# Performance work log

Measured on AMD Instinct MI355X. Metric: run time of the kernel, lower is better.

Reference implementation:

```python
import jax, jax.numpy as jnp
import numpy as np

B, C_LEN, Q_LEN, H = 32, 1024, 128, 512
NEG = -1e30  # effectively -inf for fp32 softmax


def setup_inputs() -> dict:
    key = jax.random.key(0)
    k1, k2, k3, k4, k5, k6 = jax.random.split(key, 6)
    C = jax.random.normal(k1, (B, C_LEN, H), dtype=jnp.float32)
    Q = jax.random.normal(k2, (B, Q_LEN, H), dtype=jnp.float32)
    C_mask = jax.random.randint(k3, (B, C_LEN), 0, 2, dtype=jnp.int32)
    Q_mask = jax.random.randint(k4, (B, Q_LEN), 0, 2, dtype=jnp.int32)
    # nn.Linear(3H, 1): weight [1, 3H], bias [1]; store as flat vector + scalar
    w = jax.random.normal(k5, (3 * H,), dtype=jnp.float32) * (1.0 / np.sqrt(3 * H))
    b = jax.random.normal(k6, (1,), dtype=jnp.float32) * 0.01
    return {"C": C, "Q": Q, "C_mask": C_mask, "Q_mask": Q_mask, "w": w, "b": b}


def reference(C, Q, C_mask, Q_mask, w, b):
    h = C.shape[-1]
    w1, w2, w3 = w[:h], w[h:2 * h], w[2 * h:]
    # Trilinear score decomposition (same math as Linear on cat(C, Q, C*Q)):
    # S[b,i,j] = C_i.w1 + Q_j.w2 + (C_i*w3).Q_j + bias
    S = (C @ w1)[:, :, None] + (Q @ w2)[:, None, :] \
        + jnp.einsum('bih,bjh->bij', C * w3, Q) + b[0]
    S_row = jax.nn.softmax(jnp.where(Q_mask[:, None, :] == 0, NEG, S), axis=2)
    S_col = jax.nn.softmax(jnp.where(C_mask[:, :, None] == 0, NEG, S), axis=1)
    A = jnp.einsum('bij,bjh->bih', S_row, Q)                     # [B, c_len, H]
    Bm = jnp.einsum('bij,bkj,bkh->bih', S_row, S_col, C)         # S_row @ S_col^T @ C
    return jnp.concatenate((C, A, C * A, C * Bm), axis=-1)       # [B, c_len, 4H]
```

## Files before the change

### kernel.cpp

```cpp
#include <hip/hip_runtime.h>
#include <hip/hip_bf16.h>
#include <math.h>

#define Bn 32
#define CL 1024
#define QL 128
#define Hh 512
#define NEGV (-1e30f)

typedef short bf16x8 __attribute__((ext_vector_type(8)));
typedef float f32x4 __attribute__((ext_vector_type(4)));

__device__ inline unsigned short f2bf(float x) {
  union { float f; unsigned u; } v; v.f = x;
  unsigned r = v.u + 0x7fff + ((v.u >> 16) & 1);
  return (unsigned short)(r >> 16);
}
__device__ inline unsigned packbf(float x, float y) {
  return (unsigned)f2bf(x) | ((unsigned)f2bf(y) << 16);
}

__global__ __launch_bounds__(256) void rowdot_kernel(
    const float* __restrict__ X, const float* __restrict__ w,
    const float* __restrict__ bias, float* __restrict__ out, int nrows) {
  int row = blockIdx.x * 4 + (threadIdx.x >> 6);
  int lane = threadIdx.x & 63;
  if (row >= nrows) return;
  const float* x = X + (size_t)row * Hh;
  float s = 0.f;
  for (int h = lane; h < Hh; h += 64) s += x[h] * w[h];
  for (int off = 32; off > 0; off >>= 1) s += __shfl_down(s, off, 64);
  if (lane == 0) out[row] = s + (bias ? bias[0] : 0.f);
}

__global__ __launch_bounds__(256) void prep_q_kernel(
    const float* __restrict__ Q, const float* __restrict__ w3,
    unsigned short* __restrict__ Qs, unsigned short* __restrict__ QT) {
  __shared__ float tile[QL * 65];
  int b = blockIdx.y, h0 = blockIdx.x * 64, t = threadIdx.x;
  const float* Qb = Q + (size_t)b * QL * Hh;
  unsigned* Qsu = (unsigned*)Qs + (size_t)b * QL * (Hh / 2);
  unsigned* QTu = (unsigned*)QT + ((size_t)b * Hh + h0) * (QL / 2);
  for (int l = 0; l < 16; ++l) {
    int idx = t + l * 256; int c = idx & 31, j = idx >> 5;
    float2 v = *(const float2*)(Qb + (size_t)j * Hh + h0 + 2 * c);
    float wa = w3[h0 + 2 * c], wb = w3[h0 + 2 * c + 1];
    Qsu[(size_t)j * (Hh / 2) + h0 / 2 + c] = packbf(v.x * wa, v.y * wb);
    tile[j * 65 + 2 * c] = v.x;
    tile[j * 65 + 2 * c + 1] = v.y;
  }
  __syncthreads();
  for (int l = 0; l < 16; ++l) {
    int idx = t + l * 256; int jc = idx & 63, h = idx >> 6;
    QTu[(size_t)h * (QL / 2) + jc] =
        packbf(tile[(2 * jc) * 65 + h], tile[(2 * jc + 1) * 65 + h]);
  }
}

__global__ __launch_bounds__(256) void s_mfma_kernel(
    const float* __restrict__ C, const unsigned short* __restrict__ Qs,
    const float* __restrict__ w1, const int* __restrict__ Qmask,
    const int* __restrict__ Cmask, const float* __restrict__ cq,
    float* __restrict__ S, unsigned short* __restrict__ Prow,
    unsigned short* __restrict__ C16,
    float* __restrict__ partm, float* __restrict__ partl) {
  __shared__ unsigned sA[64 * 32];
  __shared__ unsigned sB[128 * 32];
  __shared__ float rcs[64];
  __shared__ int qm[QL];
  __shared__ int cmk[64];
  __shared__ float swm[4 * QL], swl[4 * QL];
  int b = blockIdx.y, i0 = blockIdx.x * 64, t = threadIdx.x;
  if (t < QL) qm[t] = Qmask[b * QL + t];
  if (t >= 128 && t < 192) cmk[t - 128] = Cmask[b * CL + i0 + (t - 128)];
  __syncthreads();
  int lane = t & 63, w = t >> 6;
  int lanen = lane & 15, quad = lane >> 4;
  int rbase = t >> 5, cc = t & 31;
  f32x4 acc[8];
  for (int nt = 0; nt < 8; ++nt) acc[nt] = (f32x4){0.f, 0.f, 0.f, 0.f};
  float racc[8];
  for (int l = 0; l < 8; ++l) racc[l] = 0.f;
  const float* Cb = C + ((size_t)b * CL + i0) * Hh;
  unsigned* C16u = (unsigned*)C16 + ((size_t)b * CL + i0) * (Hh / 2);
  const unsigned* Qsu = (const unsigned*)Qs + (size_t)b * QL * (Hh / 2);
  for (int k0 = 0; k0 < Hh; k0 += 64) {
    float2 wv = *(const float2*)(w1 + k0 + 2 * cc);
    for (int l = 0; l < 8; ++l) {
      int rr = rbase + l * 8;
      float2 v = *(const float2*)(Cb + (size_t)rr * Hh + k0 + 2 * cc);
      unsigned pk = packbf(v.x, v.y);
      sA[rr * 32 + (cc ^ ((rr & 7) << 2))] = pk;
      C16u[(size_t)rr * (Hh / 2) + k0 / 2 + cc] = pk;
      racc[l] += v.x * wv.x + v.y * wv.y;
    }
    for (int l = 0; l < 16; ++l) {
      int idx = t + l * 256; int c = idx & 31, j = idx >> 5;
      sB[j * 32 + (c ^ ((j & 7) << 2))] = Qsu[(size_t)j * (Hh / 2) + k0 / 2 + c];
    }
    __syncthreads();
    for (int kk = 0; kk < 2; ++kk) {
      int arow = w * 16 + lanen;
      bf16x8 a = *(const bf16x8*)(sA + arow * 32 + ((kk * 16 + quad * 4) ^ ((arow & 7) << 2)));
      for (int nt = 0; nt < 8; ++nt) {
        int brow = nt * 16 + lanen;
        bf16x8 bb = *(const bf16x8*)(sB + brow * 32 + ((kk * 16 + quad * 4) ^ ((brow & 7) << 2)));
        acc[nt] = __builtin_amdgcn_mfma_f32_16x16x32_bf16(a, bb, acc[nt], 0, 0, 0);
      }
    }
    __syncthreads();
  }
  for (int l = 0; l < 8; ++l) {
    float s = racc[l];
    for (int off = 1; off <= 16; off <<= 1) s += __shfl_xor(s, off, 64);
    if (cc == 0) rcs[rbase + l * 8] = s;
  }
  __syncthreads();
  float cqv[8]; int qmv[8];
  for (int nt = 0; nt < 8; ++nt) {
    int j = nt * 16 + lanen;
    cqv[nt] = cq[b * QL + j];
    qmv[nt] = qm[j];
  }
  float colM[8], colL[8];
  for (int nt = 0; nt < 8; ++nt) { colM[nt] = -INFINITY; colL[nt] = 0.f; }
  int rowbase = i0 + w * 16 + quad * 4;
  for (int r = 0; r < 4; ++r) {
    int row = rowbase + r;
    float rcv = rcs[w * 16 + quad * 4 + r];
    int cmr = cmk[w * 16 + quad * 4 + r];
    float vals[8], mv = -INFINITY;
    for (int nt = 0; nt < 8; ++nt) {
      float val = acc[nt][r] + rcv + cqv[nt];
      vals[nt] = val;
      mv = fmaxf(mv, qmv[nt] ? val : NEGV);
    }
    for (int off = 1; off < 16; off <<= 1) mv = fmaxf(mv, __shfl_xor(mv, off, 64));
    float ls = 0.f;
    for (int nt = 0; nt < 8; ++nt) ls += __expf((qmv[nt] ? vals[nt] : NEGV) - mv);
    for (int off = 1; off < 16; off <<= 1) ls += __shfl_xor(ls, off, 64);
    float linv = 1.f / ls;
    size_t base = ((size_t)b * CL + row) * QL;
    for (int nt = 0; nt < 8; ++nt) {
      int j = nt * 16 + lanen;
      S[base + j] = vals[nt];
      Prow[base + j] = f2bf(__expf((qmv[nt] ? vals[nt] : NEGV) - mv) * linv);
      float v = cmr ? vals[nt] : NEGV;
      float nm = fmaxf(colM[nt], v);
      colL[nt] = colL[nt] * __expf(colM[nt] - nm) + __expf(v - nm);
      colM[nt] = nm;
    }
  }
  for (int off = 16; off <= 32; off <<= 1) {
    for (int nt = 0; nt < 8; ++nt) {
      float m2 = __shfl_xor(colM[nt], off, 64);
      float l2 = __shfl_xor(colL[nt], off, 64);
      float nm = fmaxf(colM[nt], m2);
      colL[nt] = colL[nt] * __expf(colM[nt] - nm) + l2 * __expf(m2 - nm);
      colM[nt] = nm;
    }
  }
  if (quad == 0) {
    for (int nt = 0; nt < 8; ++nt) {
      swm[w * QL + nt * 16 + lanen] = colM[nt];
      swl[w * QL + nt * 16 + lanen] = colL[nt];
    }
  }
  __syncthreads();
  if (t < QL) {
    float m = -INFINITY, L = 0.f;
    for (int ww = 0; ww < 4; ++ww) {
      float m2 = swm[ww * QL + t], l2 = swl[ww * QL + t];
      float nm = fmaxf(m, m2);
      L = L * __expf(m - nm) + l2 * __expf(m2 - nm);
      m = nm;
    }
    partm[((size_t)b * 16 + blockIdx.x) * QL + t] = m;
    partl[((size_t)b * 16 + blockIdx.x) * QL + t] = L;
  }
}

__global__ __launch_bounds__(128) void colstat2_kernel(
    const float* __restrict__ partm, const float* __restrict__ partl,
    float* __restrict__ colm, float* __restrict__ colinv) {
  int b = blockIdx.x, j = threadIdx.x;
  float m = -INFINITY, L = 0.f;
  for (int c = 0; c < 16; ++c) {
    float m2 = partm[(b * 16 + c) * QL + j], l2 = partl[(b * 16 + c) * QL + j];
    float nm = fmaxf(m, m2);
    L = L * __expf(m - nm) + l2 * __expf(m2 - nm);
    m = nm;
  }
  colm[b * QL + j] = m;
  colinv[b * QL + j] = 1.f / L;
}

__global__ __launch_bounds__(256) void pcol_kernel(
    const float* __restrict__ S, const int* __restrict__ Cmask,
    const float* __restrict__ colm, const float* __restrict__ colinv,
    unsigned short* __restrict__ PT) {
  __shared__ float tile[64 * 129];
  __shared__ int cm[64];
  __shared__ float cmj[QL], civ[QL];
  int b = blockIdx.y, i0 = blockIdx.x * 64, t = threadIdx.x;
  if (t < 64) cm[t] = Cmask[b * CL + i0 + t];
  if (t >= 128) { int j = t - 128; cmj[j] = colm[b * QL + j]; civ[j] = colinv[b * QL + j]; }
  __syncthreads();
  const float* Sb = S + ((size_t)b * CL + i0) * QL;
  for (int l = 0; l < 32; ++l) {
    int idx = t + l * 256; int j = idx & 127, il = idx >> 7;
    float v = cm[il] ? Sb[(size_t)il * QL + j] : NEGV;
    tile[il * 129 + j] = __expf(v - cmj[j]) * civ[j];
  }
  __syncthreads();
  unsigned* PTu = (unsigned*)PT;
  for (int l = 0; l < 16; ++l) {
    int idx = t + l * 256; int c = idx & 31, j = idx >> 5;
    PTu[(((size_t)b * QL + j) * CL + i0) / 2 + c] =
        packbf(tile[(2 * c) * 129 + j], tile[(2 * c + 1) * 129 + j]);
  }
}

__global__ __launch_bounds__(256) void t_mfma_kernel(
    const unsigned short* __restrict__ C16, const unsigned short* __restrict__ PT,
    unsigned short* __restrict__ TT) {
  __shared__ unsigned ct[64 * 17];
  __shared__ unsigned sA[32 * 32];
  __shared__ unsigned sB[128 * 32];
  int b = blockIdx.y, h0 = blockIdx.x * 32, t = threadIdx.x;
  int lane = t & 63, w = t >> 6;
  int lanen = lane & 15, quad = lane >> 4;
  int mw = w >> 1, nw = w & 1;
  f32x4 acc[4];
  for (int nt = 0; nt < 4; ++nt) acc[nt] = (f32x4){0.f, 0.f, 0.f, 0.f};
  const unsigned* C16u = (const unsigned*)C16 + (size_t)b * CL * (Hh / 2) + h0 / 2;
  const unsigned* PTu = (const unsigned*)PT + (size_t)b * QL * (CL / 2);
  const unsigned short* ct16 = (const unsigned short*)ct;
  for (int i0 = 0; i0 < CL; i0 += 64) {
    for (int l = 0; l < 4; ++l) {
      int idx = t + l * 256; int hc = idx & 15, ii = idx >> 4;
      ct[ii * 17 + hc] = C16u[(size_t)(i0 + ii) * (Hh / 2) + hc];
    }
    for (int l = 0; l < 16; ++l) {
      int idx = t + l * 256; int c = idx & 31, j = idx >> 5;
      sB[j * 32 + (c ^ ((j & 7) << 2))] = PTu[(size_t)j * (CL / 2) + i0 / 2 + c];
    }
    __syncthreads();
    for (int l = 0; l < 4; ++l) {
      int idx = t + l * 256; int c = idx & 31, hh = idx >> 5;
      unsigned lo = ct16[(2 * c) * 34 + hh];
      unsigned hi = ct16[(2 * c + 1) * 34 + hh];
      sA[hh * 32 + (c ^ ((hh & 7) << 2))] = lo | (hi << 16);
    }
    __syncthreads();
    for (int kk = 0; kk < 2; ++kk) {
      int arow = mw * 16 + lanen;
      bf16x8 a = *(const bf16x8*)(sA + arow * 32 + ((kk * 16 + quad * 4) ^ ((arow & 7) << 2)));
      for (int nt = 0; nt < 4; ++nt) {
        int brow = nw * 64 + nt * 16 + lanen;
        bf16x8 bb = *(const bf16x8*)(sB + brow * 32 + ((kk * 16 + quad * 4) ^ ((brow & 7) << 2)));
        acc[nt] = __builtin_amdgcn_mfma_f32_16x16x32_bf16(a, bb, acc[nt], 0, 0, 0);
      }
    }
    __syncthreads();
  }
  for (int nt = 0; nt < 4; ++nt)
    for (int r = 0; r < 4; ++r) {
      int h = h0 + mw * 16 + quad * 4 + r;
      int j = nw * 64 + nt * 16 + lanen;
      TT[((size_t)b * Hh + h) * QL + j] = f2bf(acc[nt][r]);
    }
}

__global__ __launch_bounds__(256) void out_mfma_kernel(
    const unsigned short* __restrict__ Prow, const unsigned short* __restrict__ TT,
    const unsigned short* __restrict__ QT, const float* __restrict__ C,
    float* __restrict__ out) {
  __shared__ unsigned sP[64 * 64];
  __shared__ unsigned sQ[64 * 64];
  __shared__ unsigned sT[64 * 64];
  int b = blockIdx.z, i0 = blockIdx.y * 64, h0 = blockIdx.x * 64, t = threadIdx.x;
  int lane = t & 63, w = t >> 6;
  int lanen = lane & 15, quad = lane >> 4;
  const unsigned* Pu = (const unsigned*)Prow + ((size_t)b * CL + i0) * (QL / 2);
  const unsigned* Tu = (const unsigned*)TT + ((size_t)b * Hh + h0) * (QL / 2);
  const unsigned* Qu = (const unsigned*)QT + ((size_t)b * Hh + h0) * (QL / 2);
  for (int l = 0; l < 16; ++l) {
    int idx = t + l * 256; int c = idx & 63, rr = idx >> 6;
    int cs = c ^ ((rr & 7) << 2);
    sP[rr * 64 + cs] = Pu[(size_t)rr * 64 + c];
    sQ[rr * 64 + cs] = Qu[(size_t)rr * 64 + c];
    sT[rr * 64 + cs] = Tu[(size_t)rr * 64 + c];
  }
  __syncthreads();
  f32x4 accA[4], accB[4];
  for (int nt = 0; nt < 4; ++nt) {
    accA[nt] = (f32x4){0.f, 0.f, 0.f, 0.f};
    accB[nt] = (f32x4){0.f, 0.f, 0.f, 0.f};
  }
  for (int kk = 0; kk < 4; ++kk) {
    int arow = w * 16 + lanen;
    bf16x8 a = *(const bf16x8*)(sP + arow * 64 + ((kk * 16 + quad * 4) ^ ((arow & 7) << 2)));
    for (int nt = 0; nt < 4; ++nt) {
      int brow = nt * 16 + lanen;
      int boff = brow * 64 + ((kk * 16 + quad * 4) ^ ((brow & 7) << 2));
      bf16x8 bq = *(const bf16x8*)(sQ + boff);
      bf16x8 bt = *(const bf16x8*)(sT + boff);
      accA[nt] = __builtin_amdgcn_mfma_f32_16x16x32_bf16(a, bq, accA[nt], 0, 0, 0);
      accB[nt] = __builtin_amdgcn_mfma_f32_16x16x32_bf16(a, bt, accB[nt], 0, 0, 0);
    }
  }
  for (int r = 0; r < 4; ++r) {
    int i = i0 + w * 16 + quad * 4 + r;
    const float* Crow = C + ((size_t)b * CL + i) * Hh;
    float* orow = out + ((size_t)b * CL + i) * (size_t)(4 * Hh);
    for (int nt = 0; nt < 4; ++nt) {
      int h = h0 + nt * 16 + lanen;
      float cv = Crow[h];
      float av = accA[nt][r], bv = accB[nt][r];
      orow[h] = cv;
      orow[Hh + h] = av;
      orow[2 * Hh + h] = cv * av;
      orow[3 * Hh + h] = cv * bv;
    }
  }
}

extern "C" void kernel_launch(void* const* d_in, const int* in_sizes, int n_in,
                              void* d_out, int out_size, void* d_ws, size_t ws_size,
                              hipStream_t stream) {
  const float* C = (const float*)d_in[0];
  const float* Q = (const float*)d_in[1];
  const int* Cmask = (const int*)d_in[2];
  const int* Qmask = (const int*)d_in[3];
  const float* w = (const float*)d_in[4];
  const float* bptr = (const float*)d_in[5];
  float* out = (float*)d_out;
  float* f = (float*)d_ws;

  float* cq     = f;
  float* colm   = f + 4096;
  float* colinv = f + 8192;
  float* partm  = f + 12288;
  float* partl  = f + 77824;
  float* S      = f + 143360;
  unsigned short* Prow = (unsigned short*)(f + 4337664);
  unsigned short* PT   = Prow + 4194304;
  unsigned short* TT   = PT + 4194304;
  unsigned short* C16  = TT + 2097152;
  unsigned short* Qs   = C16 + 16777216;
  unsigned short* QT   = Qs + 2097152;

  rowdot_kernel<<<dim3((Bn * QL) / 4), 256, 0, stream>>>(Q, w + Hh, bptr, cq, Bn * QL);
  prep_q_kernel<<<dim3(Hh / 64, Bn), 256, 0, stream>>>(Q, w + 2 * Hh, Qs, QT);
  s_mfma_kernel<<<dim3(CL / 64, Bn), 256, 0, stream>>>(C, Qs, w, Qmask, Cmask, cq, S,
                                                       Prow, C16, partm, partl);
  colstat2_kernel<<<dim3(Bn), 128, 0, stream>>>(partm, partl, colm, colinv);
  pcol_kernel<<<dim3(CL / 64, Bn), 256, 0, stream>>>(S, Cmask, colm, colinv, PT);
  t_mfma_kernel<<<dim3(Hh / 32, Bn), 256, 0, stream>>>(C16, PT, TT);
  out_mfma_kernel<<<dim3(Hh / 64, CL / 64, Bn), 256, 0, stream>>>(Prow, TT, QT, C, out);
}
```

Measured before the change: 538.8 us.

## Split C prep into own kernel, store S in fp16, coalesce output stores via LDS

A new prep_c kernel converts C to bf16 and computes the C·w1 row dot products with vectorised loads. The S-score kernel then reads bf16 C directly instead of converting it inline. The intermediate score matrix S is stored as fp16 instead of fp32, halving its write and read traffic, and pcol now stages bf16 values in LDS. The output kernel stages its MFMA accumulators through shared memory so each wave writes contiguous 64-float rows. The fp16 rounding of S adds precision risk for the column softmax, and the extra kernel adds a launch plus one more pass over C.

```diff
diff --git a/kernel.cpp b/kernel.cpp
--- a/kernel.cpp
+++ b/kernel.cpp
@@ -1,5 +1,6 @@
 #include <hip/hip_runtime.h>
 #include <hip/hip_bf16.h>
+#include <hip/hip_fp16.h>
 #include <math.h>
 
 #define Bn 32
@@ -18,6 +19,31 @@
 }
 __device__ inline unsigned packbf(float x, float y) {
   return (unsigned)f2bf(x) | ((unsigned)f2bf(y) << 16);
+}
+
+__global__ __launch_bounds__(256) void prep_c_kernel(
+    const float* __restrict__ C, const float* __restrict__ w1,
+    float* __restrict__ rc, unsigned short* __restrict__ C16) {
+  int t = threadIdx.x;
+  int row = blockIdx.x * 16 + (t >> 4);
+  int seg = t & 15;
+  const float* x = C + (size_t)row * Hh + seg * 32;
+  unsigned* y = (unsigned*)C16 + (size_t)row * (Hh / 2) + seg * 16;
+  float s = 0.f;
+  for (int q = 0; q < 4; ++q) {
+    float4 v0 = *(const float4*)(x + q * 8);
+    float4 v1 = *(const float4*)(x + q * 8 + 4);
+    float4 w0 = *(const float4*)(w1 + seg * 32 + q * 8);
+    float4 w1v = *(const float4*)(w1 + seg * 32 + q * 8 + 4);
+    s += v0.x * w0.x + v0.y * w0.y + v0.z * w0.z + v0.w * w0.w;
+    s += v1.x * w1v.x + v1.y * w1v.y + v1.z * w1v.z + v1.w * w1v.w;
+    uint4 st;
+    st.x = packbf(v0.x, v0.y); st.y = packbf(v0.z, v0.w);
+    st.z = packbf(v1.x, v1.y); st.w = packbf(v1.z, v1.w);
+    *(uint4*)(y + q * 4) = st;
+  }
+  for (int off = 1; off < 16; off <<= 1) s += __shfl_xor(s, off, 64);
+  if (seg == 0) rc[row] = s;
 }
 
 __global__ __launch_bounds__(256) void rowdot_kernel(
@@ -58,15 +84,13 @@
 }
 
 __global__ __launch_bounds__(256) void s_mfma_kernel(
-    const float* __restrict__ C, const unsigned short* __restrict__ Qs,
-    const float* __restrict__ w1, const int* __restrict__ Qmask,
-    const int* __restrict__ Cmask, const float* __restrict__ cq,
-    float* __restrict__ S, unsigned short* __restrict__ Prow,
-    unsigned short* __restrict__ C16,
+    const unsigned short* __restrict__ C16, const unsigned short* __restrict__ Qs,
+    const int* __restrict__ Qmask, const int* __restrict__ Cmask,
+    const float* __restrict__ rc, const float* __restrict__ cq,
+    unsigned short* __restrict__ S16, unsigned short* __restrict__ Prow,
     float* __restrict__ partm, float* __restrict__ partl) {
   __shared__ unsigned sA[64 * 32];
   __shared__ unsigned sB[128 * 32];
-  __shared__ float rcs[64];
   __shared__ int qm[QL];
   __shared__ int cmk[64];
   __shared__ float swm[4 * QL], swl[4 * QL];
@@ -76,27 +100,19 @@
   __syncthreads();
   int lane = t & 63, w = t >> 6;
   int lanen = lane & 15, quad = lane >> 4;
-  int rbase = t >> 5, cc = t & 31;
+  int c = t & 31, rA = t >> 5;
   f32x4 acc[8];
   for (int nt = 0; nt < 8; ++nt) acc[nt] = (f32x4){0.f, 0.f, 0.f, 0.f};
-  float racc[8];
-  for (int l = 0; l < 8; ++l) racc[l] = 0.f;
-  const float* Cb = C + ((size_t)b * CL + i0) * Hh;
-  unsigned* C16u = (unsigned*)C16 + ((size_t)b * CL + i0) * (Hh / 2);
-  const unsigned* Qsu = (const unsigned*)Qs + (size_t)b * QL * (Hh / 2);
-  for (int k0 = 0; k0 < Hh; k0 += 64) {
-    float2 wv = *(const float2*)(w1 + k0 + 2 * cc);
+  const unsigned* Cu = (const unsigned*)C16 + ((size_t)b * CL + i0) * (Hh / 2);
+  const unsigned* Qu = (const unsigned*)Qs + (size_t)b * QL * (Hh / 2);
+  for (int k0 = 0; k0 < Hh / 2; k0 += 32) {
     for (int l = 0; l < 8; ++l) {
-      int rr = rbase + l * 8;
-      float2 v = *(const float2*)(Cb + (size_t)rr * Hh + k0 + 2 * cc);
-      unsigned pk = packbf(v.x, v.y);
-      sA[rr * 32 + (cc ^ ((rr & 7) << 2))] = pk;
-      C16u[(size_t)rr * (Hh / 2) + k0 / 2 + cc] = pk;
-      racc[l] += v.x * wv.x + v.y * wv.y;
+      int rr = rA + l * 8;
+      sA[rr * 32 + (c ^ ((rr & 7) << 2))] = Cu[(size_t)rr * (Hh / 2) + k0 + c];
     }
     for (int l = 0; l < 16; ++l) {
-      int idx = t + l * 256; int c = idx & 31, j = idx >> 5;
-      sB[j * 32 + (c ^ ((j & 7) << 2))] = Qsu[(size_t)j * (Hh / 2) + k0 / 2 + c];
+      int idx = t + l * 256; int cc = idx & 31, j = idx >> 5;
+      sB[j * 32 + (cc ^ ((j & 7) << 2))] = Qu[(size_t)j * (Hh / 2) + k0 + cc];
     }
     __syncthreads();
     for (int kk = 0; kk < 2; ++kk) {
@@ -110,24 +126,17 @@
     }
     __syncthreads();
   }
-  for (int l = 0; l < 8; ++l) {
-    float s = racc[l];
-    for (int off = 1; off <= 16; off <<= 1) s += __shfl_xor(s, off, 64);
-    if (cc == 0) rcs[rbase + l * 8] = s;
-  }
-  __syncthreads();
   float cqv[8]; int qmv[8];
   for (int nt = 0; nt < 8; ++nt) {
     int j = nt * 16 + lanen;
-    cqv[nt] = cq[b * QL + j];
-    qmv[nt] = qm[j];
+    cqv[nt] = cq[b * QL + j]; qmv[nt] = qm[j];
   }
   float colM[8], colL[8];
   for (int nt = 0; nt < 8; ++nt) { colM[nt] = -INFINITY; colL[nt] = 0.f; }
   int rowbase = i0 + w * 16 + quad * 4;
   for (int r = 0; r < 4; ++r) {
     int row = rowbase + r;
-    float rcv = rcs[w * 16 + quad * 4 + r];
+    float rcv = rc[b * CL + row];
     int cmr = cmk[w * 16 + quad * 4 + r];
     float vals[8], mv = -INFINITY;
     for (int nt = 0; nt < 8; ++nt) {
@@ -143,7 +152,7 @@
     size_t base = ((size_t)b * CL + row) * QL;
     for (int nt = 0; nt < 8; ++nt) {
       int j = nt * 16 + lanen;
-      S[base + j] = vals[nt];
+      S16[base + j] = __half_as_ushort(__float2half(vals[nt]));
       Prow[base + j] = f2bf(__expf((qmv[nt] ? vals[nt] : NEGV) - mv) * linv);
       float v = cmr ? vals[nt] : NEGV;
       float nm = fmaxf(colM[nt], v);
@@ -196,28 +205,32 @@
 }
 
 __global__ __launch_bounds__(256) void pcol_kernel(
-    const float* __restrict__ S, const int* __restrict__ Cmask,
+    const unsigned short* __restrict__ S16, const int* __restrict__ Cmask,
     const float* __restrict__ colm, const float* __restrict__ colinv,
     unsigned short* __restrict__ PT) {
-  __shared__ float tile[64 * 129];
+  __shared__ unsigned short tile[64 * 130];
   __shared__ int cm[64];
   __shared__ float cmj[QL], civ[QL];
   int b = blockIdx.y, i0 = blockIdx.x * 64, t = threadIdx.x;
   if (t < 64) cm[t] = Cmask[b * CL + i0 + t];
   if (t >= 128) { int j = t - 128; cmj[j] = colm[b * QL + j]; civ[j] = colinv[b * QL + j]; }
   __syncthreads();
-  const float* Sb = S + ((size_t)b * CL + i0) * QL;
-  for (int l = 0; l < 32; ++l) {
-    int idx = t + l * 256; int j = idx & 127, il = idx >> 7;
-    float v = cm[il] ? Sb[(size_t)il * QL + j] : NEGV;
-    tile[il * 129 + j] = __expf(v - cmj[j]) * civ[j];
+  const unsigned* Su = (const unsigned*)S16 + ((size_t)b * CL + i0) * (QL / 2);
+  for (int l = 0; l < 16; ++l) {
+    int idx = t + l * 256; int jc = idx & 63, il = idx >> 6;
+    unsigned v = Su[(size_t)il * 64 + jc];
+    int j0 = jc * 2;
+    float v0 = cm[il] ? __half2float(__ushort_as_half((unsigned short)(v & 0xffff))) : NEGV;
+    float v1 = cm[il] ? __half2float(__ushort_as_half((unsigned short)(v >> 16))) : NEGV;
+    tile[il * 130 + j0]     = f2bf(__expf(v0 - cmj[j0]) * civ[j0]);
+    tile[il * 130 + j0 + 1] = f2bf(__expf(v1 - cmj[j0 + 1]) * civ[j0 + 1]);
   }
   __syncthreads();
   unsigned* PTu = (unsigned*)PT;
   for (int l = 0; l < 16; ++l) {
-    int idx = t + l * 256; int c = idx & 31, j = idx >> 5;
-    PTu[(((size_t)b * QL + j) * CL + i0) / 2 + c] =
-        packbf(tile[(2 * c) * 129 + j], tile[(2 * c + 1) * 129 + j]);
+    int idx = t + l * 256; int ci = idx & 31, j = idx >> 5;
+    PTu[(((size_t)b * QL + j) * CL + i0) / 2 + ci] =
+        (unsigned)tile[(2 * ci) * 130 + j] | ((unsigned)tile[(2 * ci + 1) * 130 + j] << 16);
   }
 }
 
@@ -233,24 +246,24 @@
   int mw = w >> 1, nw = w & 1;
   f32x4 acc[4];
   for (int nt = 0; nt < 4; ++nt) acc[nt] = (f32x4){0.f, 0.f, 0.f, 0.f};
-  const unsigned* C16u = (const unsigned*)C16 + (size_t)b * CL * (Hh / 2) + h0 / 2;
+  const unsigned* Cu = (const unsigned*)C16 + (size_t)b * CL * (Hh / 2) + h0 / 2;
   const unsigned* PTu = (const unsigned*)PT + (size_t)b * QL * (CL / 2);
   const unsigned short* ct16 = (const unsigned short*)ct;
   for (int i0 = 0; i0 < CL; i0 += 64) {
     for (int l = 0; l < 4; ++l) {
       int idx = t + l * 256; int hc = idx & 15, ii = idx >> 4;
-      ct[ii * 17 + hc] = C16u[(size_t)(i0 + ii) * (Hh / 2) + hc];
+      ct[ii * 17 + hc] = Cu[(size_t)(i0 + ii) * (Hh / 2) + hc];
     }
     for (int l = 0; l < 16; ++l) {
-      int idx = t + l * 256; int c = idx & 31, j = idx >> 5;
-      sB[j * 32 + (c ^ ((j & 7) << 2))] = PTu[(size_t)j * (CL / 2) + i0 / 2 + c];
+      int idx = t + l * 256; int c2 = idx & 31, j = idx >> 5;
+      sB[j * 32 + (c2 ^ ((j & 7) << 2))] = PTu[(size_t)j * (CL / 2) + i0 / 2 + c2];
     }
     __syncthreads();
     for (int l = 0; l < 4; ++l) {
-      int idx = t + l * 256; int c = idx & 31, hh = idx >> 5;
-      unsigned lo = ct16[(2 * c) * 34 + hh];
-      unsigned hi = ct16[(2 * c + 1) * 34 + hh];
-      sA[hh * 32 + (c ^ ((hh & 7) << 2))] = lo | (hi << 16);
+      int idx = t + l * 256; int c2 = idx & 31, hh = idx >> 5;
+      unsigned lo = ct16[(2 * c2) * 34 + hh];
+      unsigned hi = ct16[(2 * c2 + 1) * 34 + hh];
+      sA[hh * 32 + (c2 ^ ((hh & 7) << 2))] = lo | (hi << 16);
     }
     __syncthreads();
     for (int kk = 0; kk < 2; ++kk) {
@@ -276,9 +289,10 @@
     const unsigned short* __restrict__ Prow, const unsigned short* __restrict__ TT,
     const unsigned short* __restrict__ QT, const float* __restrict__ C,
     float* __restrict__ out) {
-  __shared__ unsigned sP[64 * 64];
-  __shared__ unsigned sQ[64 * 64];
-  __shared__ unsigned sT[64 * 64];
+  __shared__ unsigned smem[3 * 64 * 64];
+  unsigned* sP = smem;
+  unsigned* sQ = smem + 64 * 64;
+  unsigned* sT = smem + 2 * 64 * 64;
   int b = blockIdx.z, i0 = blockIdx.y * 64, h0 = blockIdx.x * 64, t = threadIdx.x;
   int lane = t & 63, w = t >> 6;
   int lanen = lane & 15, quad = lane >> 4;
@@ -310,19 +324,29 @@
       accB[nt] = __builtin_amdgcn_mfma_f32_16x16x32_bf16(a, bt, accB[nt], 0, 0, 0);
     }
   }
-  for (int r = 0; r < 4; ++r) {
-    int i = i0 + w * 16 + quad * 4 + r;
-    const float* Crow = C + ((size_t)b * CL + i) * Hh;
-    float* orow = out + ((size_t)b * CL + i) * (size_t)(4 * Hh);
-    for (int nt = 0; nt < 4; ++nt) {
-      int h = h0 + nt * 16 + lanen;
-      float cv = Crow[h];
-      float av = accA[nt][r], bv = accB[nt][r];
-      orow[h] = cv;
-      orow[Hh + h] = av;
-      orow[2 * Hh + h] = cv * av;
-      orow[3 * Hh + h] = cv * bv;
-    }
+  __syncthreads();
+  float* fA = (float*)smem;
+  float* fB = (float*)smem + 64 * 65;
+  for (int nt = 0; nt < 4; ++nt)
+    for (int r = 0; r < 4; ++r) {
+      int iL = w * 16 + quad * 4 + r;
+      int hL = nt * 16 + lanen;
+      fA[iL * 65 + hL] = accA[nt][r];
+      fB[iL * 65 + hL] = accB[nt][r];
+    }
+  __syncthreads();
+  for (int rr = 0; rr < 16; ++rr) {
+    int iL = w * 16 + rr;
+    int i = i0 + iL;
+    const float* Crow = C + ((size_t)b * CL + i) * Hh + h0;
+    float* orow = out + ((size_t)b * CL + i) * (size_t)(4 * Hh) + h0;
+    float cv = Crow[lane];
+    float av = fA[iL * 65 + lane];
+    float bv = fB[iL * 65 + lane];
+    orow[lane] = cv;
+    orow[Hh + lane] = av;
+    orow[2 * Hh + lane] = cv * av;
+    orow[3 * Hh + lane] = cv * bv;
   }
 }
 
@@ -338,25 +362,28 @@
   float* out = (float*)d_out;
   float* f = (float*)d_ws;
 
-  float* cq     = f;
-  float* colm   = f + 4096;
-  float* colinv = f + 8192;
-  float* partm  = f + 12288;
-  float* partl  = f + 77824;
-  float* S      = f + 143360;
-  unsigned short* Prow = (unsigned short*)(f + 4337664);
+  float* rc     = f;
+  float* cq     = f + 32768;
+  float* colm   = f + 36864;
+  float* colinv = f + 40960;
+  float* partm  = f + 45056;
+  float* partl  = f + 110592;
+  unsigned short* u = (unsigned short*)(f + 176128);
+  unsigned short* S16  = u;
+  unsigned short* Prow = S16 + 4194304;
   unsigned short* PT   = Prow + 4194304;
   unsigned short* TT   = PT + 4194304;
-  unsigned short* C16  = TT + 2097152;
-  unsigned short* Qs   = C16 + 16777216;
-  unsigned short* QT   = Qs + 2097152;
-
+  unsigned short* QT   = TT + 2097152;
+  unsigned short* Qs   = QT + 2097152;
+  unsigned short* C16  = Qs + 2097152;
+
+  prep_c_kernel<<<dim3((Bn * CL) / 16), 256, 0, stream>>>(C, w, rc, C16);
   rowdot_kernel<<<dim3((Bn * QL) / 4), 256, 0, stream>>>(Q, w + Hh, bptr, cq, Bn * QL);
   prep_q_kernel<<<dim3(Hh / 64, Bn), 256, 0, stream>>>(Q, w + 2 * Hh, Qs, QT);
-  s_mfma_kernel<<<dim3(CL / 64, Bn), 256, 0, stream>>>(C, Qs, w, Qmask, Cmask, cq, S,
-                                                       Prow, C16, partm, partl);
+  s_mfma_kernel<<<dim3(CL / 64, Bn), 256, 0, stream>>>(C16, Qs, Qmask, Cmask, rc, cq,
+                                                       S16, Prow, partm, partl);
   colstat2_kernel<<<dim3(Bn), 128, 0, stream>>>(partm, partl, colm, colinv);
-  pcol_kernel<<<dim3(CL / 64, Bn), 256, 0, stream>>>(S, Cmask, colm, colinv, PT);
+  pcol_kernel<<<dim3(CL / 64, Bn), 256, 0, stream>>>(S16, Cmask, colm, colinv, PT);
   t_mfma_kernel<<<dim3(Hh / 32, Bn), 256, 0, stream>>>(C16, PT, TT);
   out_mfma_kernel<<<dim3(Hh / 64, CL / 64, Bn), 256, 0, stream>>>(Prow, TT, QT, C, out);
 }
```

Measured after the change: 536.7 us. Within noise of the previous version (-0.4%).
